# Kernel optimization log

Measured on AMD Instinct MI355X. Metric: run time of the kernel, lower is better.

The kernel has to match this reference:

```python
import jax, jax.numpy as jnp
import numpy as np

N_NODES = 50000
NODE_DIM = 256
HIDDEN = 512
N_EDGES = 500000


def setup_inputs() -> dict:
    key = jax.random.key(0)
    k1, k2, k3, k4 = jax.random.split(key, 4)
    x = jax.random.normal(k1, (N_NODES, NODE_DIM), dtype=jnp.float32)
    edge_index = jax.random.randint(k2, (2, N_EDGES), 0, N_NODES, dtype=jnp.int64)
    in_dim = 2 * NODE_DIM  # concat mode
    W1 = jax.random.normal(k3, (in_dim, HIDDEN), dtype=jnp.float32) / np.sqrt(in_dim)
    b1 = jnp.zeros((HIDDEN,), dtype=jnp.float32)
    W2 = jax.random.normal(k4, (HIDDEN, 1), dtype=jnp.float32) / np.sqrt(HIDDEN)
    b2 = jnp.zeros((1,), dtype=jnp.float32)
    return {"x": x, "edge_index": edge_index, "W1": W1, "b1": b1, "W2": W2, "b2": b2}


def reference(x, edge_index, W1, b1, W2, b2):
    row, col = edge_index[0], edge_index[1]
    # concat mode: edge_feat [E, 2*node_dim]
    edge_feat = jnp.concatenate([x[row], x[col]], axis=1)
    h = jax.nn.relu(edge_feat @ W1 + b1)  # [E, hidden]
    score = (h @ W2 + b2).squeeze(-1)     # [E]
    return score
```

## Files before the change

### kernel.cpp

```cpp
#include <hip/hip_runtime.h>
#include <hip/hip_bf16.h>

#define N_NODES  50000
#define NODE_DIM 256
#define HIDDEN   512
#define N_EDGES  500000
#define M_PAD    50048
#define NCAT     1024
#define KDIM     256
#define NB       391
#define CAP      1536
#define NSLOTS   (NB * CAP)
#define QSCALE   30.238095f
#define DSCALE   0.033070866f
#define DUMMY    0xFFFFFFFF00000000ULL

typedef __attribute__((ext_vector_type(8))) unsigned short ushort8;
typedef __attribute__((ext_vector_type(4))) unsigned short ushort4v;
typedef __attribute__((ext_vector_type(8))) __bf16 bf16x8;
typedef __attribute__((ext_vector_type(4))) float f32x4;
typedef __attribute__((ext_vector_type(4))) unsigned int uint4v;
typedef __attribute__((ext_vector_type(2))) unsigned int uint2v;
typedef __attribute__((ext_vector_type(2))) unsigned long long ull2;

__device__ __forceinline__ unsigned short f2bf(float f) {
  unsigned int u = __builtin_bit_cast(unsigned int, f);
  u += 0x7fffu + ((u >> 16) & 1u);
  return (unsigned short)(u >> 16);
}

__device__ __forceinline__ void gload16(const void* g, void* l) {
  __builtin_amdgcn_global_load_lds(
      (__attribute__((address_space(1))) void*)(g),
      (__attribute__((address_space(3))) void*)(l),
      16, 0, 0);
}

__global__ void prep_kernel(const float* __restrict__ x, unsigned short* __restrict__ xb,
                            const float* __restrict__ W1, unsigned short* __restrict__ wt,
                            int* __restrict__ counts, unsigned long long* __restrict__ slots) {
  const int b = blockIdx.x;
  if (b < 2048) {
    const int total4 = M_PAD * NODE_DIM / 4;
    const int valid4 = N_NODES * NODE_DIM / 4;
    for (int i = b * 256 + threadIdx.x; i < total4; i += 2048 * 256) {
      ushort4v o;
      if (i < valid4) {
        float4 v = ((const float4*)x)[i];
        o[0] = f2bf(v.x); o[1] = f2bf(v.y); o[2] = f2bf(v.z); o[3] = f2bf(v.w);
      } else {
        o[0] = 0; o[1] = 0; o[2] = 0; o[3] = 0;
      }
      ((ushort4v*)xb)[i] = o;
    }
  } else if (b < 3072) {
    int i = (b - 2048) * 256 + threadIdx.x;
    int n = i >> 8;
    int k = i & 255;
    int srow = (n >= HIDDEN) ? (NODE_DIM + k) : k;
    int scol = n & (HIDDEN - 1);
    wt[i] = f2bf(W1[srow * HIDDEN + scol]);
  } else if (b == 3072) {
    for (int i = threadIdx.x; i < NB; i += 256) counts[i] = 0;
  } else {
    int bb = b - 3073;
    for (int i = bb * 256 + threadIdx.x; i < NSLOTS; i += 512 * 256)
      slots[i] = DUMMY;
  }
}

__global__ __launch_bounds__(256, 2) void gemm_kernel(
    const unsigned short* __restrict__ Xb,
    const unsigned short* __restrict__ Wt,
    const float* __restrict__ b1,
    unsigned short* __restrict__ CbA,
    signed char* __restrict__ CbB) {
  __shared__ unsigned short As[128 * 32];
  __shared__ unsigned short Bs[128 * 32];
  const int t = threadIdx.x;
  const int w = t >> 6;
  const int lane = t & 63;
  const int bid = blockIdx.x;
  const int tileM = bid >> 3;
  const int tileN = bid & 7;
  const int wm = w >> 1, wn = w & 1;

  f32x4 acc[4][4] = {};

  const int rowA0 = tileM * 128;
  const int rowB0 = tileN * 128;
  const int rstage = t >> 2;
  const int cstage = (t & 3) * 8;

  for (int kk = 0; kk < KDIM; kk += 32) {
#pragma unroll
    for (int i = 0; i < 2; ++i) {
      const unsigned short* srcA = Xb + (size_t)(rowA0 + i * 64 + rstage) * KDIM + kk + cstage;
      gload16(srcA, (char*)As + i * 4096 + w * 1024);
      const unsigned short* srcB = Wt + (size_t)(rowB0 + i * 64 + rstage) * KDIM + kk + cstage;
      gload16(srcB, (char*)Bs + i * 4096 + w * 1024);
    }
    __syncthreads();

    bf16x8 a[4], bfr[4];
#pragma unroll
    for (int fm = 0; fm < 4; ++fm)
      a[fm] = *(const bf16x8*)&As[(wm * 64 + fm * 16 + (lane & 15)) * 32 + (lane >> 4) * 8];
#pragma unroll
    for (int fn = 0; fn < 4; ++fn)
      bfr[fn] = *(const bf16x8*)&Bs[(wn * 64 + fn * 16 + (lane & 15)) * 32 + (lane >> 4) * 8];
#pragma unroll
    for (int fm = 0; fm < 4; ++fm)
#pragma unroll
      for (int fn = 0; fn < 4; ++fn)
        acc[fm][fn] = __builtin_amdgcn_mfma_f32_16x16x32_bf16(a[fm], bfr[fn], acc[fm][fn], 0, 0, 0);
    __syncthreads();
  }

  const int row0 = tileM * 128 + wm * 64;
  if (tileN < 4) {
    const int col0 = tileN * 128 + wn * 64;
    float b1v[4];
#pragma unroll
    for (int fn = 0; fn < 4; ++fn) b1v[fn] = b1[col0 + fn * 16 + (lane & 15)];
#pragma unroll
    for (int fm = 0; fm < 4; ++fm)
#pragma unroll
      for (int fn = 0; fn < 4; ++fn)
#pragma unroll
        for (int r = 0; r < 4; ++r) {
          int row = row0 + fm * 16 + (lane >> 4) * 4 + r;
          int col = col0 + fn * 16 + (lane & 15);
          CbA[(size_t)row * HIDDEN + col] = f2bf(acc[fm][fn][r] + b1v[fn]);
        }
  } else {
    const int col0 = (tileN - 4) * 128 + wn * 64;
#pragma unroll
    for (int fm = 0; fm < 4; ++fm)
#pragma unroll
      for (int fn = 0; fn < 4; ++fn)
#pragma unroll
        for (int r = 0; r < 4; ++r) {
          int row = row0 + fm * 16 + (lane >> 4) * 4 + r;
          int col = col0 + fn * 16 + (lane & 15);
          float v = fminf(fmaxf(acc[fm][fn][r], -4.2f), 4.2f);
          CbB[(size_t)row * HIDDEN + col] = (signed char)__float2int_rn(v * QSCALE);
        }
  }
}

__global__ void scatter_kernel(const int* __restrict__ ei, int* __restrict__ counts,
                               unsigned long long* __restrict__ slots) {
  __shared__ int h[NB];
  __shared__ int bbase[NB];
  const int chunk = (N_EDGES + gridDim.x - 1) / gridDim.x;
  const int e0 = blockIdx.x * chunk;
  const int e1 = min(e0 + chunk, N_EDGES);
  for (int i = threadIdx.x; i < NB; i += blockDim.x) h[i] = 0;
  __syncthreads();
  for (int e = e0 + threadIdx.x; e < e1; e += blockDim.x)
    atomicAdd(&h[ei[e] >> 7], 1);
  __syncthreads();
  for (int i = threadIdx.x; i < NB; i += blockDim.x) {
    int c = h[i];
    bbase[i] = c ? atomicAdd(&counts[i], c) : 0;
    h[i] = 0;
  }
  __syncthreads();
  for (int e = e0 + threadIdx.x; e < e1; e += blockDim.x) {
    int r = ei[e];
    int c = ei[N_EDGES + e];
    int b = r >> 7;
    int idx = bbase[b] + atomicAdd(&h[b], 1);
    slots[(size_t)b * CAP + idx] =
        (unsigned long long)r | ((unsigned long long)c << 16) | ((unsigned long long)e << 32);
  }
}

__device__ __forceinline__ float edge_mlp(uint4v ua, uint2v ub, const float* w2r) {
  float acc = 0.f;
#pragma unroll
  for (int j = 0; j < 4; ++j) {
    float alo = __builtin_bit_cast(float, ua[j] << 16);
    float ahi = __builtin_bit_cast(float, ua[j] & 0xffff0000u);
    unsigned int ubw = ub[j >> 1];
    int sh = (j & 1) * 16;
    int qlo = (int)(signed char)(ubw >> sh);
    int qhi = (int)(signed char)(ubw >> (sh + 8));
    float hlo = fmaxf(fmaf((float)qlo, DSCALE, alo), 0.f);
    float hhi = fmaxf(fmaf((float)qhi, DSCALE, ahi), 0.f);
    acc = fmaf(hlo, w2r[2 * j], acc);
    acc = fmaf(hhi, w2r[2 * j + 1], acc);
  }
  return acc;
}

__global__ __launch_bounds__(256) void edge_kernel(
    const unsigned short* __restrict__ CbA,
    const signed char* __restrict__ CbB,
    const unsigned long long* __restrict__ slots,
    const float* __restrict__ W2,
    const float* __restrict__ b2,
    float* __restrict__ out) {
  const int lane = threadIdx.x & 63;
  const int xcd = blockIdx.x & 7;
  const int lwid = (blockIdx.x >> 3) * 4 + (threadIdx.x >> 6);
  const int nlw = (gridDim.x >> 3) * 4;
  const int per_xcd = NSLOTS / 8;
  const int pbase = xcd * per_xcd;
  const int base = lane * 8;

  float w2r[8];
  {
    float4 u0 = *(const float4*)&W2[base];
    float4 u1 = *(const float4*)&W2[base + 4];
    w2r[0] = u0.x; w2r[1] = u0.y; w2r[2] = u0.z; w2r[3] = u0.w;
    w2r[4] = u1.x; w2r[5] = u1.y; w2r[6] = u1.z; w2r[7] = u1.w;
  }
  const float bias2 = b2[0];

  const int pend = pbase + per_xcd;
  for (int p = pbase + lwid * 2; p < pend; p += nlw * 2) {
    ull2 rr = *(const ull2*)(slots + p);
    const int id0 = (int)(rr[0] >> 32);
    const int id1 = (int)(rr[1] >> 32);
    if ((id0 & id1) < 0) continue;
    const int r0 = (int)(rr[0] & 0xFFFF), c0 = (int)((rr[0] >> 16) & 0xFFFF);
    const int r1 = (int)(rr[1] & 0xFFFF), c1 = (int)((rr[1] >> 16) & 0xFFFF);
    uint4v ua0 = *(const uint4v*)(CbA + (size_t)r0 * HIDDEN + base);
    uint2v ub0 = *(const uint2v*)(CbB + (size_t)c0 * HIDDEN + base);
    uint4v ua1 = *(const uint4v*)(CbA + (size_t)r1 * HIDDEN + base);
    uint2v ub1 = *(const uint2v*)(CbB + (size_t)c1 * HIDDEN + base);

    float acc0 = edge_mlp(ua0, ub0, w2r);
    float acc1 = edge_mlp(ua1, ub1, w2r);
#pragma unroll
    for (int off = 32; off; off >>= 1) {
      acc0 += __shfl_xor(acc0, off, 64);
      acc1 += __shfl_xor(acc1, off, 64);
    }
    if (lane == 0) {
      if (id0 >= 0) out[id0] = acc0 + bias2;
      if (id1 >= 0) out[id1] = acc1 + bias2;
    }
  }
}

extern "C" void kernel_launch(void* const* d_in, const int* in_sizes, int n_in,
                              void* d_out, int out_size, void* d_ws, size_t ws_size,
                              hipStream_t stream) {
  const float* x  = (const float*)d_in[0];
  const int*   ei = (const int*)d_in[1];
  const float* W1 = (const float*)d_in[2];
  const float* b1 = (const float*)d_in[3];
  const float* W2 = (const float*)d_in[4];
  const float* b2 = (const float*)d_in[5];
  float* out = (float*)d_out;

  char* ws = (char*)d_ws;
  const size_t xb_bytes  = (size_t)M_PAD * KDIM * 2;
  const size_t wt_bytes  = (size_t)NCAT * KDIM * 2;
  const size_t cbA_bytes = (size_t)M_PAD * HIDDEN * 2;
  const size_t cbB_bytes = (size_t)M_PAD * HIDDEN;
  unsigned short* xb  = (unsigned short*)ws;
  unsigned short* wt  = (unsigned short*)(ws + xb_bytes);
  unsigned short* cbA = (unsigned short*)(ws + xb_bytes + wt_bytes);
  signed char*    cbB = (signed char*)(ws + xb_bytes + wt_bytes + cbA_bytes);
  char* tail = ws + xb_bytes + wt_bytes + cbA_bytes + cbB_bytes;
  int* counts = (int*)tail;
  unsigned long long* slots = (unsigned long long*)(tail + 4096);

  hipLaunchKernelGGL(prep_kernel, dim3(3585), dim3(256), 0, stream, x, xb, W1, wt, counts, slots);
  hipLaunchKernelGGL(gemm_kernel, dim3((M_PAD / 128) * (NCAT / 128)), dim3(256), 0, stream,
                     xb, wt, b1, cbA, cbB);
  hipLaunchKernelGGL(scatter_kernel, dim3(512), dim3(256), 0, stream, ei, counts, slots);
  hipLaunchKernelGGL(edge_kernel, dim3(2048), dim3(256), 0, stream, cbA, cbB, slots, W2, b2, out);
}
```

Baseline: 154.8 us.

## Split wave into four 16-lane groups, one edge per group in edge kernel

Reorganizes the edge scoring kernel so that each 64-lane wave handles four edges at once, with each 16-lane quarter covering one edge and each lane processing 32 hidden units instead of 8. Loads become wider per lane (four 16-byte bf16 loads plus two 16-byte int8 loads), and the cross-lane reduction drops from six shuffle steps to four. The aim is fewer shuffles per edge and more memory parallelism per wave, at the cost of more registers per lane (32 W2 weights, larger load buffers), which may reduce occupancy.

After: 160.8 us. 1.04x slower.

```diff
diff --git a/kernel.cpp b/kernel.cpp
--- a/kernel.cpp
+++ b/kernel.cpp
@@ -177,24 +177,6 @@
   }
 }
 
-__device__ __forceinline__ float edge_mlp(uint4v ua, uint2v ub, const float* w2r) {
-  float acc = 0.f;
-#pragma unroll
-  for (int j = 0; j < 4; ++j) {
-    float alo = __builtin_bit_cast(float, ua[j] << 16);
-    float ahi = __builtin_bit_cast(float, ua[j] & 0xffff0000u);
-    unsigned int ubw = ub[j >> 1];
-    int sh = (j & 1) * 16;
-    int qlo = (int)(signed char)(ubw >> sh);
-    int qhi = (int)(signed char)(ubw >> (sh + 8));
-    float hlo = fmaxf(fmaf((float)qlo, DSCALE, alo), 0.f);
-    float hhi = fmaxf(fmaf((float)qhi, DSCALE, ahi), 0.f);
-    acc = fmaf(hlo, w2r[2 * j], acc);
-    acc = fmaf(hhi, w2r[2 * j + 1], acc);
-  }
-  return acc;
-}
-
 __global__ __launch_bounds__(256) void edge_kernel(
     const unsigned short* __restrict__ CbA,
     const signed char* __restrict__ CbB,
@@ -203,46 +185,53 @@
     const float* __restrict__ b2,
     float* __restrict__ out) {
   const int lane = threadIdx.x & 63;
+  const int q = lane >> 4;
+  const int sub = lane & 15;
   const int xcd = blockIdx.x & 7;
   const int lwid = (blockIdx.x >> 3) * 4 + (threadIdx.x >> 6);
   const int nlw = (gridDim.x >> 3) * 4;
   const int per_xcd = NSLOTS / 8;
   const int pbase = xcd * per_xcd;
-  const int base = lane * 8;
-
-  float w2r[8];
-  {
-    float4 u0 = *(const float4*)&W2[base];
-    float4 u1 = *(const float4*)&W2[base + 4];
-    w2r[0] = u0.x; w2r[1] = u0.y; w2r[2] = u0.z; w2r[3] = u0.w;
-    w2r[4] = u1.x; w2r[5] = u1.y; w2r[6] = u1.z; w2r[7] = u1.w;
-  }
+
+  float w2r[32];
+#pragma unroll
+  for (int i = 0; i < 8; ++i)
+    *(float4*)&w2r[i * 4] = *(const float4*)(W2 + sub * 32 + i * 4);
   const float bias2 = b2[0];
-
   const int pend = pbase + per_xcd;
-  for (int p = pbase + lwid * 2; p < pend; p += nlw * 2) {
-    ull2 rr = *(const ull2*)(slots + p);
-    const int id0 = (int)(rr[0] >> 32);
-    const int id1 = (int)(rr[1] >> 32);
-    if ((id0 & id1) < 0) continue;
-    const int r0 = (int)(rr[0] & 0xFFFF), c0 = (int)((rr[0] >> 16) & 0xFFFF);
-    const int r1 = (int)(rr[1] & 0xFFFF), c1 = (int)((rr[1] >> 16) & 0xFFFF);
-    uint4v ua0 = *(const uint4v*)(CbA + (size_t)r0 * HIDDEN + base);
-    uint2v ub0 = *(const uint2v*)(CbB + (size_t)c0 * HIDDEN + base);
-    uint4v ua1 = *(const uint4v*)(CbA + (size_t)r1 * HIDDEN + base);
-    uint2v ub1 = *(const uint2v*)(CbB + (size_t)c1 * HIDDEN + base);
-
-    float acc0 = edge_mlp(ua0, ub0, w2r);
-    float acc1 = edge_mlp(ua1, ub1, w2r);
-#pragma unroll
-    for (int off = 32; off; off >>= 1) {
-      acc0 += __shfl_xor(acc0, off, 64);
-      acc1 += __shfl_xor(acc1, off, 64);
+
+  for (int p = pbase + lwid * 4; p < pend; p += nlw * 4) {
+    const unsigned long long rec = slots[p + q];
+    const int id = (int)(rec >> 32);
+    if (__all(id < 0)) continue;
+    const int r = (int)(rec & 0xFFFF);
+    const int c = (int)((rec >> 16) & 0xFFFF);
+    const uint4v* pa = (const uint4v*)(CbA + (size_t)r * HIDDEN + sub * 32);
+    const uint4v* pb = (const uint4v*)(CbB + (size_t)c * HIDDEN + sub * 32);
+    uint4v ua[4];
+    ua[0] = pa[0]; ua[1] = pa[1]; ua[2] = pa[2]; ua[3] = pa[3];
+    uint4v ub[2];
+    ub[0] = pb[0]; ub[1] = pb[1];
+
+    float acc = 0.f;
+#pragma unroll
+    for (int j = 0; j < 16; ++j) {
+      unsigned int au = ua[j >> 2][j & 3];
+      float alo = __builtin_bit_cast(float, au << 16);
+      float ahi = __builtin_bit_cast(float, au & 0xffff0000u);
+      unsigned int ubw = ub[j >> 3][(j >> 1) & 3];
+      int sh = (j & 1) * 16;
+      int qlo = (int)(signed char)(ubw >> sh);
+      int qhi = (int)(signed char)(ubw >> (sh + 8));
+      float hlo = fmaxf(fmaf((float)qlo, DSCALE, alo), 0.f);
+      float hhi = fmaxf(fmaf((float)qhi, DSCALE, ahi), 0.f);
+      acc = fmaf(hlo, w2r[2 * j], acc);
+      acc = fmaf(hhi, w2r[2 * j + 1], acc);
     }
-    if (lane == 0) {
-      if (id0 >= 0) out[id0] = acc0 + bias2;
-      if (id1 >= 0) out[id1] = acc1 + bias2;
-    }
+#pragma unroll
+    for (int off = 8; off; off >>= 1)
+      acc += __shfl_xor(acc, off, 64);
+    if (sub == 0 && id >= 0) out[id] = acc + bias2;
   }
 }
 
```
